# Optimization experiments

Measured on AMD Instinct MI355X. Metric: run time of the kernel, lower is better.

## Reference

```python
import jax, jax.numpy as jnp
import numpy as np

N_IN, N_HID, N_OUT = 200, 256, 2
BN_EPS = 1e-5


def _mlp(x, W1, b1, W2, b2):
    # two-layer MLP with ELU activations (dropout prob = 0.0 -> omitted)
    h = jax.nn.elu(x @ W1 + b1)
    return jax.nn.elu(h @ W2 + b2)


def _batch_norm(x, gamma, beta):
    # torch BatchNorm1d in training mode over flattened (B*E) rows, biased variance
    m = x.mean(axis=(0, 1))
    v = x.var(axis=(0, 1))
    return (x - m) * jax.lax.rsqrt(v + BN_EPS) * gamma + beta


def setup_inputs() -> dict:
    key = jax.random.key(0)
    ks = jax.random.split(key, 12)
    B, N, T, D = 32, 100, 50, 4
    inputs = jax.random.normal(ks[0], (B, N, T, D), dtype=jnp.float32)
    # one-hot receiver/sender matrices over all N*(N-1) ordered off-diagonal pairs
    idx = np.array([(i, j) for i in range(N) for j in range(N) if i != j])
    eye = np.eye(N, dtype=np.float32)
    rel_rec = jnp.asarray(eye[idx[:, 0]])   # [E, N]
    rel_send = jnp.asarray(eye[idx[:, 1]])  # [E, N]

    def lin(k, fi, fo):  # xavier_normal weight
        std = float(np.sqrt(2.0 / (fi + fo)))
        return jax.random.normal(k, (fi, fo), dtype=jnp.float32) * std

    b = lambda n: jnp.full((n,), 0.1, dtype=jnp.float32)
    return dict(
        inputs=inputs, rel_rec=rel_rec, rel_send=rel_send,
        mlp1_W1=lin(ks[1], N_IN, N_HID), mlp1_b1=b(N_HID),
        mlp1_W2=lin(ks[2], N_HID, N_HID), mlp1_b2=b(N_HID),
        mlp2_W1=lin(ks[3], 2 * N_HID, N_HID), mlp2_b1=b(N_HID),
        mlp2_W2=lin(ks[4], N_HID, N_HID), mlp2_b2=b(N_HID),
        mlp3_W1=lin(ks[5], N_HID, N_HID), mlp3_b1=b(N_HID),
        mlp3_W2=lin(ks[6], N_HID, N_HID), mlp3_b2=b(N_HID),
        mlp4_W1=lin(ks[7], 3 * N_HID, N_HID), mlp4_b1=b(N_HID),
        mlp4_W2=lin(ks[8], N_HID, N_HID), mlp4_b2=b(N_HID),
        mlp4_bn_gamma=jnp.ones((N_HID,), jnp.float32),
        mlp4_bn_beta=jnp.zeros((N_HID,), jnp.float32),
        fc_W=lin(ks[9], N_HID, N_OUT), fc_b=b(N_OUT),
    )


def reference(inputs, rel_rec, rel_send,
              mlp1_W1, mlp1_b1, mlp1_W2, mlp1_b2,
              mlp2_W1, mlp2_b1, mlp2_W2, mlp2_b2,
              mlp3_W1, mlp3_b1, mlp3_W2, mlp3_b2,
              mlp4_W1, mlp4_b1, mlp4_W2, mlp4_b2,
              mlp4_bn_gamma, mlp4_bn_beta, fc_W, fc_b):
    B, N = inputs.shape[0], inputs.shape[1]
    x = inputs.reshape(B, N, -1)                       # [B, N, T*D]
    x = _mlp(x, mlp1_W1, mlp1_b1, mlp1_W2, mlp1_b2)     # [B, N, H]

    def node2edge(h):
        recv = jnp.einsum('en,bnh->beh', rel_rec, h)
        send = jnp.einsum('en,bnh->beh', rel_send, h)
        return jnp.concatenate([send, recv], axis=2)    # [B, E, 2H]

    x = node2edge(x)
    x = _mlp(x, mlp2_W1, mlp2_b1, mlp2_W2, mlp2_b2)     # [B, E, H]
    x_skip = x
    # factor=True branch
    incoming = jnp.einsum('en,beh->bnh', rel_rec, x) / x.shape[1]  # edge2node, /N per code
    x = _mlp(incoming, mlp3_W1, mlp3_b1, mlp3_W2, mlp3_b2)
    x = node2edge(x)                                    # [B, E, 2H]
    x = jnp.concatenate([x, x_skip], axis=2)            # [B, E, 3H]
    x = _mlp(x, mlp4_W1, mlp4_b1, mlp4_W2, mlp4_b2)
    x = _batch_norm(x, mlp4_bn_gamma, mlp4_bn_beta)
    return x @ fc_W + fc_b                              # [B, E, n_out]
```

## Files before the change

kernel.cpp:

```cpp
#include <hip/hip_runtime.h>
#include <math.h>


typedef unsigned short ushort_t;
typedef __bf16 bf16x8 __attribute__((ext_vector_type(8)));
typedef float  f32x4  __attribute__((ext_vector_type(4)));

#define E_EDGES 9900
#define NNODE   100
#define HID     256
#define M_BIG   316800
#define M_SMALL 3200
#define NBLK2   (M_BIG / 128)

__device__ __forceinline__ float bf2f(ushort_t u) {
    union { unsigned int i; float f; } v; v.i = ((unsigned int)u) << 16; return v.f;
}
__device__ __forceinline__ ushort_t f2bf(float f) {
    union { float f; unsigned int i; } v; v.f = f;
    return (ushort_t)((v.i + 0x7fffu + ((v.i >> 16) & 1u)) >> 16);
}
__device__ __forceinline__ float elu_f(float x) {
    return x > 0.f ? x : (__expf(x) - 1.f);
}

__global__ __launch_bounds__(256)
void wcvt_all(const float* __restrict__ s0, const float* __restrict__ s1,
              const float* __restrict__ s2, const float* __restrict__ s3,
              const float* __restrict__ s4, const float* __restrict__ s5,
              const float* __restrict__ s6, const float* __restrict__ s7,
              ushort_t* d0, ushort_t* d1, ushort_t* d2, ushort_t* d3,
              ushort_t* d4, ushort_t* d5, ushort_t* d6, ushort_t* d7)
{
    int bid = blockIdx.x;
    const float* S; ushort_t* D; int Kd, Kr, t;
    if      (bid < 16)  { S = s0; D = d0; Kd = 256; Kr = 200; t = bid; }
    else if (bid < 32)  { S = s1; D = d1; Kd = 256; Kr = 256; t = bid - 16; }
    else if (bid < 64)  { S = s2; D = d2; Kd = 512; Kr = 512; t = bid - 32; }
    else if (bid < 80)  { S = s3; D = d3; Kd = 256; Kr = 256; t = bid - 64; }
    else if (bid < 96)  { S = s4; D = d4; Kd = 256; Kr = 256; t = bid - 80; }
    else if (bid < 112) { S = s5; D = d5; Kd = 256; Kr = 256; t = bid - 96; }
    else if (bid < 160) { S = s6; D = d6; Kd = 768; Kr = 768; t = bid - 112; }
    else                { S = s7; D = d7; Kd = 256; Kr = 256; t = bid - 160; }
    int k0 = (t >> 2) * 64, c0 = (t & 3) * 64;
    __shared__ float Sh[64][65];
    int tid = threadIdx.x;
    #pragma unroll
    for (int i = 0; i < 16; ++i) {
        int idx = tid + i * 256;
        int kk = idx >> 6, cc = idx & 63;
        Sh[kk][cc] = (k0 + kk < Kr) ? S[(size_t)(k0 + kk) * 256 + c0 + cc] : 0.f;
    }
    __syncthreads();
    int col = tid & 63;
    int kb  = (tid >> 6) * 16;
    ushort_t* dst = D + (size_t)(c0 + col) * Kd + k0 + kb;
    #pragma unroll
    for (int jj = 0; jj < 4; ++jj) {
        ushort4 u;
        u.x = f2bf(Sh[kb + 4 * jj + 0][col]);
        u.y = f2bf(Sh[kb + 4 * jj + 1][col]);
        u.z = f2bf(Sh[kb + 4 * jj + 2][col]);
        u.w = f2bf(Sh[kb + 4 * jj + 3][col]);
        *(ushort4*)(dst + 4 * jj) = u;
    }
}

__device__ __forceinline__ void gemm32(const ushort_t S[32][264],
                                       const ushort_t* __restrict__ WT,
                                       int wstr, int kcn,
                                       int w, int ln15, int klane,
                                       f32x4 acc[2][4])
{
    #pragma unroll
    for (int r = 0; r < 2; ++r)
        #pragma unroll
        for (int c = 0; c < 4; ++c)
            acc[r][c][0] = acc[r][c][1] = acc[r][c][2] = acc[r][c][3] = 0.f;
    int wch[4];
    #pragma unroll
    for (int c = 0; c < 4; ++c) wch[c] = (w * 64 + 16 * c + ln15) * wstr;
    bf16x8 wf0[4];
    #pragma unroll
    for (int c = 0; c < 4; ++c)
        wf0[c] = *(const bf16x8*)(WT + wch[c] + klane);
    for (int kc = 0; kc < kcn; ++kc) {
        bf16x8 wf1[4];
        if (kc + 1 < kcn) {
            #pragma unroll
            for (int c = 0; c < 4; ++c)
                wf1[c] = *(const bf16x8*)(WT + wch[c] + (kc + 1) * 32 + klane);
        }
        bf16x8 af[2];
        #pragma unroll
        for (int r = 0; r < 2; ++r)
            af[r] = *(const bf16x8*)&S[16 * r + ln15][kc * 32 + klane];
        #pragma unroll
        for (int r = 0; r < 2; ++r)
            #pragma unroll
            for (int c = 0; c < 4; ++c)
                acc[r][c] = __builtin_amdgcn_mfma_f32_16x16x32_bf16(wf0[c], af[r], acc[r][c], 0, 0, 0);
        #pragma unroll
        for (int c = 0; c < 4; ++c) wf0[c] = wf1[c];
    }
}

__device__ __forceinline__ void park32(ushort_t D[32][264], f32x4 acc[2][4],
                                       const float* __restrict__ bias,
                                       int act, int w, int ln15, int q)
{
    #pragma unroll
    for (int c = 0; c < 4; ++c) {
        float4 bv = bias ? *(const float4*)&bias[w * 64 + 16 * c + 4 * q]
                         : make_float4(0.f, 0.f, 0.f, 0.f);
        #pragma unroll
        for (int r = 0; r < 2; ++r) {
            float o0 = acc[r][c][0] + bv.x;
            float o1 = acc[r][c][1] + bv.y;
            float o2 = acc[r][c][2] + bv.z;
            float o3 = acc[r][c][3] + bv.w;
            if (act) { o0 = elu_f(o0); o1 = elu_f(o1); o2 = elu_f(o2); o3 = elu_f(o3); }
            ushort4 u;
            u.x = f2bf(o0); u.y = f2bf(o1); u.z = f2bf(o2); u.w = f2bf(o3);
            *(ushort4*)&D[16 * r + ln15][w * 64 + 16 * c + 4 * q] = u;
        }
    }
}

__global__ __launch_bounds__(256, 4)
void mlp_pq(const float* __restrict__ Xf, int Kreal, int kcN, float xscale,
            const ushort_t* __restrict__ W1T, const float* __restrict__ b1,
            const ushort_t* __restrict__ W2T, const float* __restrict__ b2,
            const ushort_t* __restrict__ WPT, int wsPQ,
            const float* __restrict__ bP, ushort_t* __restrict__ Pout,
            const ushort_t* __restrict__ WQT, ushort_t* __restrict__ Qout)
{
    __shared__ ushort_t Abuf[32][264];
    __shared__ ushort_t Bbuf[32][264];
    const int tid = threadIdx.x;
    const int w = tid >> 6;
    const int l = tid & 63;
    const int ln15 = l & 15;
    const int q = l >> 4;
    const int klane = 8 * q;
    const int Rbase = blockIdx.x * 32;

    {
        int row = tid >> 3, seg = tid & 7;
        if (seg < kcN) {
            ushort_t tmp[32];
            const float* src = Xf + (size_t)(Rbase + row) * Kreal + seg * 32;
            #pragma unroll
            for (int u = 0; u < 32; ++u)
                tmp[u] = (seg * 32 + u < Kreal) ? f2bf(src[u] * xscale) : (ushort_t)0;
            #pragma unroll
            for (int u = 0; u < 4; ++u)
                *(uint4*)&Abuf[row][seg * 32 + u * 8] = *(uint4*)&tmp[u * 8];
        }
    }
    __syncthreads();

    f32x4 acc[2][4];
    gemm32(Abuf, W1T, 256, kcN, w, ln15, klane, acc);
    park32(Bbuf, acc, b1, 1, w, ln15, q);
    __syncthreads();
    gemm32(Bbuf, W2T, 256, 8, w, ln15, klane, acc);
    park32(Abuf, acc, b2, 1, w, ln15, q);
    __syncthreads();
    gemm32(Abuf, WPT, wsPQ, 8, w, ln15, klane, acc);
    park32(Bbuf, acc, bP, 0, w, ln15, q);
    __syncthreads();
    f32x4 acq[2][4];
    gemm32(Abuf, WQT, wsPQ, 8, w, ln15, klane, acq);
    #pragma unroll
    for (int m = 0; m < 4; ++m) {
        int ch = tid + m * 256;
        int row = ch >> 5;
        int o = (ch & 31) * 8;
        *(uint4*)&Pout[(size_t)(Rbase + row) * 256 + o] = *(const uint4*)&Bbuf[row][o];
    }
    __syncthreads();
    park32(Bbuf, acq, nullptr, 0, w, ln15, q);
    __syncthreads();
    #pragma unroll
    for (int m = 0; m < 4; ++m) {
        int ch = tid + m * 256;
        int row = ch >> 5;
        int o = (ch & 31) * 8;
        *(uint4*)&Qout[(size_t)(Rbase + row) * 256 + o] = *(const uint4*)&Bbuf[row][o];
    }
}

__device__ __forceinline__ void gemm128cs(const ushort_t As[128][264],
                                          const ushort_t* __restrict__ WT,
                                          int wstr, int w, int ln15, int klane,
                                          f32x4 acc[8][2])
{
    #pragma unroll
    for (int r = 0; r < 8; ++r)
        #pragma unroll
        for (int c = 0; c < 2; ++c)
            acc[r][c][0] = acc[r][c][1] = acc[r][c][2] = acc[r][c][3] = 0.f;
    int wch[2];
    #pragma unroll
    for (int c = 0; c < 2; ++c) wch[c] = (w * 32 + 16 * c + ln15) * wstr;
    bf16x8 wf0[2];
    #pragma unroll
    for (int c = 0; c < 2; ++c)
        wf0[c] = *(const bf16x8*)(WT + wch[c] + klane);
    #pragma unroll
    for (int kc = 0; kc < 8; ++kc) {
        bf16x8 wf1[2];
        if (kc < 7) {
            #pragma unroll
            for (int c = 0; c < 2; ++c)
                wf1[c] = *(const bf16x8*)(WT + wch[c] + (kc + 1) * 32 + klane);
        }
        #pragma unroll
        for (int g = 0; g < 2; ++g) {
            bf16x8 af[4];
            #pragma unroll
            for (int r = 0; r < 4; ++r)
                af[r] = *(const bf16x8*)&As[16 * (4 * g + r) + ln15][kc * 32 + klane];
            #pragma unroll
            for (int r = 0; r < 4; ++r)
                #pragma unroll
                for (int c = 0; c < 2; ++c)
                    acc[4 * g + r][c] = __builtin_amdgcn_mfma_f32_16x16x32_bf16(wf0[c], af[r], acc[4 * g + r][c], 0, 0, 0);
        }
        #pragma unroll
        for (int c = 0; c < 2; ++c) wf0[c] = wf1[c];
    }
}

__global__ __launch_bounds__(512, 4)
void edge_mlp2(const ushort_t* __restrict__ Pb, const ushort_t* __restrict__ Qb,
               const ushort_t* __restrict__ W2T,
               const float* __restrict__ b2,
               ushort_t* __restrict__ Y, float* __restrict__ aux)
{
    __shared__ ushort_t As[128][264];
    const int tid = threadIdx.x;
    const int w = tid >> 6;
    const int l = tid & 63;
    const int ln15 = l & 15;
    const int q = l >> 4;
    const int klane = 8 * q;
    const int Rbase = blockIdx.x * 128;

    {
        int row = tid >> 2;
        int R = Rbase + row;
        int b = R / E_EDGES;
        int e = R - b * E_EDGES;
        int i = e / 99;
        int k = e - 99 * i;
        int j = k + (k >= i ? 1 : 0);
        const ushort_t* prow = Pb + (size_t)(b * NNODE + j) * HID;
        const ushort_t* qrow = Qb + (size_t)(b * NNODE + i) * HID;
        int off = (tid & 3) * 8;
        uint4 pv[8], qv[8];
        #pragma unroll
        for (int u = 0; u < 8; ++u) {
            int o = off + u * 32;
            pv[u] = *(const uint4*)(prow + o);
            qv[u] = *(const uint4*)(qrow + o);
        }
        #pragma unroll
        for (int u = 0; u < 8; ++u) {
            int o = off + u * 32;
            union { uint4 v; ushort_t s[8]; } pu, qu, hu;
            pu.v = pv[u]; qu.v = qv[u];
            #pragma unroll
            for (int x = 0; x < 8; ++x)
                hu.s[x] = f2bf(elu_f(bf2f(pu.s[x]) + bf2f(qu.s[x])));
            *(uint4*)&As[row][o] = hu.v;
        }
    }
    __syncthreads();

    f32x4 acc[8][2];
    gemm128cs(As, W2T, 256, w, ln15, klane, acc);
    __syncthreads();

    #pragma unroll
    for (int c = 0; c < 2; ++c) {
        float4 bv = *(const float4*)&b2[w * 32 + 16 * c + 4 * q];
        #pragma unroll
        for (int r = 0; r < 8; ++r) {
            ushort4 u;
            u.x = f2bf(elu_f(acc[r][c][0] + bv.x));
            u.y = f2bf(elu_f(acc[r][c][1] + bv.y));
            u.z = f2bf(elu_f(acc[r][c][2] + bv.z));
            u.w = f2bf(elu_f(acc[r][c][3] + bv.w));
            *(ushort4*)&As[16 * r + ln15][w * 32 + 16 * c + 4 * q] = u;
        }
    }
    __syncthreads();

    #pragma unroll
    for (int m = 0; m < 8; ++m) {
        int ch = tid + m * 512;
        int row = ch >> 5;
        int o = (ch & 31) * 8;
        *(uint4*)&Y[((size_t)(Rbase + row)) * 256 + o] = *(const uint4*)&As[row][o];
    }

    if (tid < 64) {
        int c4 = tid * 4;
        int bn = Rbase / 99;
        int left = 99 - (Rbase - bn * 99);
        float s[4] = {0.f, 0.f, 0.f, 0.f};
        for (int r = 0; r < 128; ++r) {
            union { ushort4 v; ushort_t e[4]; } u;
            u.v = *(const ushort4*)&As[r][c4];
            #pragma unroll
            for (int g = 0; g < 4; ++g) s[g] += bf2f(u.e[g]);
            if (--left == 0) {
                #pragma unroll
                for (int g = 0; g < 4; ++g) {
                    atomicAdd(&aux[(size_t)bn * 256 + c4 + g], s[g]);
                    s[g] = 0.f;
                }
                ++bn; left = 99;
            }
        }
        #pragma unroll
        for (int g = 0; g < 4; ++g)
            atomicAdd(&aux[(size_t)bn * 256 + c4 + g], s[g]);
    }
}

__global__ __launch_bounds__(512, 4)
void edge_mlp4(const ushort_t* __restrict__ Pb, const ushort_t* __restrict__ Qb,
               const ushort_t* __restrict__ X2,
               const ushort_t* __restrict__ WaT, int wsA,
               const ushort_t* __restrict__ WbT, int wsB,
               const float* __restrict__ b2,
               ushort_t* __restrict__ Y, ushort_t* __restrict__ pstat)
{
    __shared__ ushort_t As[128][264];
    const int tid = threadIdx.x;
    const int w = tid >> 6;
    const int l = tid & 63;
    const int ln15 = l & 15;
    const int q = l >> 4;
    const int klane = 8 * q;
    const int Rbase = blockIdx.x * 128;

    {
        int row = tid >> 2;
        const ushort_t* xrow = X2 + (size_t)(Rbase + row) * 256;
        int off = (tid & 3) * 8;
        uint4 xv[8];
        #pragma unroll
        for (int u = 0; u < 8; ++u) xv[u] = *(const uint4*)(xrow + off + u * 32);
        #pragma unroll
        for (int u = 0; u < 8; ++u) *(uint4*)&As[row][off + u * 32] = xv[u];
    }

    int oP[8], oQ[8];
    #pragma unroll
    for (int r = 0; r < 8; ++r) {
        int R = Rbase + 16 * r + ln15;
        int b = R / E_EDGES;
        int e = R - b * E_EDGES;
        int i = e / 99;
        int k = e - 99 * i;
        int j = k + (k >= i ? 1 : 0);
        oP[r] = (b * NNODE + j) * HID;
        oQ[r] = (b * NNODE + i) * HID;
    }
    __syncthreads();

    f32x4 acc[8][2];
    gemm128cs(As, WaT, wsA, w, ln15, klane, acc);
    __syncthreads();

    #pragma unroll
    for (int c = 0; c < 2; ++c) {
        int ch = w * 32 + 16 * c + 4 * q;
        ushort4 pv[8], qv[8];
        #pragma unroll
        for (int r = 0; r < 8; ++r) {
            pv[r] = *(const ushort4*)(Pb + oP[r] + ch);
            qv[r] = *(const ushort4*)(Qb + oQ[r] + ch);
        }
        #pragma unroll
        for (int r = 0; r < 8; ++r) {
            union { ushort4 v; ushort_t s[4]; } pu, qu;
            pu.v = pv[r]; qu.v = qv[r];
            ushort4 u;
            u.x = f2bf(elu_f(acc[r][c][0] + bf2f(pu.s[0]) + bf2f(qu.s[0])));
            u.y = f2bf(elu_f(acc[r][c][1] + bf2f(pu.s[1]) + bf2f(qu.s[1])));
            u.z = f2bf(elu_f(acc[r][c][2] + bf2f(pu.s[2]) + bf2f(qu.s[2])));
            u.w = f2bf(elu_f(acc[r][c][3] + bf2f(pu.s[3]) + bf2f(qu.s[3])));
            *(ushort4*)&As[16 * r + ln15][ch] = u;
        }
    }
    __syncthreads();

    gemm128cs(As, WbT, wsB, w, ln15, klane, acc);
    __syncthreads();

    #pragma unroll
    for (int c = 0; c < 2; ++c) {
        float4 bv = *(const float4*)&b2[w * 32 + 16 * c + 4 * q];
        #pragma unroll
        for (int r = 0; r < 8; ++r) {
            ushort4 u;
            u.x = f2bf(elu_f(acc[r][c][0] + bv.x));
            u.y = f2bf(elu_f(acc[r][c][1] + bv.y));
            u.z = f2bf(elu_f(acc[r][c][2] + bv.z));
            u.w = f2bf(elu_f(acc[r][c][3] + bv.w));
            *(ushort4*)&As[16 * r + ln15][w * 32 + 16 * c + 4 * q] = u;
        }
    }
    __syncthreads();

    #pragma unroll
    for (int m = 0; m < 8; ++m) {
        int ch = tid + m * 512;
        int row = ch >> 5;
        int o = (ch & 31) * 8;
        *(uint4*)&Y[((size_t)(Rbase + row)) * 256 + o] = *(const uint4*)&As[row][o];
    }

    if (tid < 64) {
        int c4 = tid * 4;
        float s[4] = {0.f, 0.f, 0.f, 0.f};
        float qq[4] = {0.f, 0.f, 0.f, 0.f};
        for (int r = 0; r < 128; ++r) {
            union { ushort4 v; ushort_t e[4]; } u;
            u.v = *(const ushort4*)&As[r][c4];
            #pragma unroll
            for (int g = 0; g < 4; ++g) {
                float v = bf2f(u.e[g]);
                s[g] += v;
                qq[g] = fmaf(v, v, qq[g]);
            }
        }
        size_t base = (size_t)blockIdx.x * 512;
        ushort4 us, uq;
        us.x = f2bf(s[0]);  us.y = f2bf(s[1]);  us.z = f2bf(s[2]);  us.w = f2bf(s[3]);
        uq.x = f2bf(qq[0]); uq.y = f2bf(qq[1]); uq.z = f2bf(qq[2]); uq.w = f2bf(qq[3]);
        *(ushort4*)&pstat[base + c4]       = us;
        *(ushort4*)&pstat[base + 256 + c4] = uq;
    }
}

__global__ __launch_bounds__(256)
void reduce_stats(const ushort_t* __restrict__ pstat, float* __restrict__ stats)
{
    int c = threadIdx.x;
    float s = 0.f, q = 0.f;
    for (int b = blockIdx.x; b < NBLK2; b += 64) {
        size_t base = (size_t)b * 512;
        s += bf2f(pstat[base + c]);
        q += bf2f(pstat[base + 256 + c]);
    }
    atomicAdd(&stats[c], s);
    atomicAdd(&stats[256 + c], q);
}

__global__ __launch_bounds__(256)
void fold_kernel(const float* __restrict__ stats,
                 const float* __restrict__ gamma, const float* __restrict__ beta,
                 const float* __restrict__ fcW, const float* __restrict__ fcb,
                 float* __restrict__ fold)
{
    __shared__ float red0[256], red1[256];
    int c = threadIdx.x;
    float mean  = stats[c] * (1.f / M_BIG);
    float var   = stats[256 + c] * (1.f / M_BIG) - mean * mean;
    float inv   = rsqrtf(var + 1e-5f);
    float scale = inv * gamma[c];
    float sh    = beta[c] - mean * scale;
    float w0 = fcW[c * 2 + 0], w1 = fcW[c * 2 + 1];
    fold[c * 2 + 0] = scale * w0;
    fold[c * 2 + 1] = scale * w1;
    red0[c] = sh * w0;
    red1[c] = sh * w1;
    __syncthreads();
    for (int off = 128; off > 0; off >>= 1) {
        if (c < off) { red0[c] += red0[c + off]; red1[c] += red1[c + off]; }
        __syncthreads();
    }
    if (c == 0) {
        fold[512] = red0[0] + fcb[0];
        fold[513] = red1[0] + fcb[1];
    }
}

__global__ __launch_bounds__(256)
void final_kernel(const ushort_t* __restrict__ x4, const float* __restrict__ fold,
                  float* __restrict__ out)
{
    int tid  = threadIdx.x;
    int l32  = tid & 31;
    int g    = tid >> 5;
    int R = blockIdx.x * 8 + g;
    int c0 = l32 * 8;
    union { uint4 qv; ushort_t s[8]; } u;
    u.qv = *(const uint4*)(x4 + (size_t)R * 256 + c0);
    float a0 = 0.f, a1 = 0.f;
    #pragma unroll
    for (int j = 0; j < 8; ++j) {
        float v = bf2f(u.s[j]);
        a0 = fmaf(v, fold[(c0 + j) * 2 + 0], a0);
        a1 = fmaf(v, fold[(c0 + j) * 2 + 1], a1);
    }
    #pragma unroll
    for (int off = 16; off > 0; off >>= 1) {
        a0 += __shfl_down(a0, off);
        a1 += __shfl_down(a1, off);
    }
    if (l32 == 0) {
        out[(size_t)R * 2 + 0] = a0 + fold[512];
        out[(size_t)R * 2 + 1] = a1 + fold[513];
    }
}

extern "C" void kernel_launch(void* const* d_in, const int* in_sizes, int n_in,
                              void* d_out, int out_size, void* d_ws, size_t ws_size,
                              hipStream_t stream)
{
    (void)in_sizes; (void)n_in; (void)out_size; (void)ws_size;

    const float* inputs = (const float*)d_in[0];
    const float* m1W1 = (const float*)d_in[3];
    const float* m1b1 = (const float*)d_in[4];
    const float* m1W2 = (const float*)d_in[5];
    const float* m1b2 = (const float*)d_in[6];
    const float* m2W1 = (const float*)d_in[7];
    const float* m2b1 = (const float*)d_in[8];
    const float* m2W2 = (const float*)d_in[9];
    const float* m2b2 = (const float*)d_in[10];
    const float* m3W1 = (const float*)d_in[11];
    const float* m3b1 = (const float*)d_in[12];
    const float* m3W2 = (const float*)d_in[13];
    const float* m3b2 = (const float*)d_in[14];
    const float* m4W1 = (const float*)d_in[15];
    const float* m4b1 = (const float*)d_in[16];
    const float* m4W2 = (const float*)d_in[17];
    const float* m4b2 = (const float*)d_in[18];
    const float* gamma = (const float*)d_in[19];
    const float* beta  = (const float*)d_in[20];
    const float* fcW   = (const float*)d_in[21];
    const float* fcb   = (const float*)d_in[22];
    float* out = (float*)d_out;

    char* ws = (char*)d_ws;
    const size_t BIGB = (size_t)M_BIG * 256 * 2;
    const size_t HB   = (size_t)M_SMALL * 256 * 2;
    const size_t SM4  = (size_t)M_SMALL * 256 * 4;
    ushort_t* bigX     = (ushort_t*)ws;
    ushort_t* pstat    = (ushort_t*)(ws + BIGB);
    float*    incoming = (float*)(ws + BIGB + 2 * HB);
    ushort_t* Pbuf     = (ushort_t*)(ws + BIGB + 2 * HB + SM4);
    ushort_t* Qbuf     = (ushort_t*)(ws + BIGB + 3 * HB + SM4);
    float*    stats    = (float*)(ws + BIGB + 4 * HB + SM4);
    float*    fold     = stats + 512;
    ushort_t* w1t      = (ushort_t*)(ws + BIGB + 4 * HB + SM4 + 8192);
    ushort_t* w1bt     = w1t  + 256 * 256;
    ushort_t* w2pt     = w1bt + 256 * 256;
    ushort_t* w2t      = w2pt + 256 * 512;
    ushort_t* w3at     = w2t  + 256 * 256;
    ushort_t* w3bt     = w3at + 256 * 256;
    ushort_t* w4pt     = w3bt + 256 * 256;
    ushort_t* w4bt     = w4pt + 256 * 768;

    hipMemsetAsync(stats, 0, 2048, stream);
    hipMemsetAsync(incoming, 0, SM4, stream);

    dim3 blk(256);
    dim3 blk512(512);
    wcvt_all<<<176, blk, 0, stream>>>(m1W1, m1W2, m2W1, m2W2, m3W1, m3W2, m4W1, m4W2,
                                      w1t, w1bt, w2pt, w2t, w3at, w3bt, w4pt, w4bt);
    mlp_pq<<<100, blk, 0, stream>>>(inputs, 200, 7, 1.f,
                                    w1t, m1b1, w1bt, m1b2,
                                    w2pt, 512, m2b1, Pbuf,
                                    w2pt + 256, Qbuf);
    edge_mlp2<<<NBLK2, blk512, 0, stream>>>(Pbuf, Qbuf, w2t, m2b2, bigX, incoming);
    mlp_pq<<<100, blk, 0, stream>>>(incoming, 256, 8, 1.f / 9900.f,
                                    w3at, m3b1, w3bt, m3b2,
                                    w4pt, 768, m4b1, Pbuf,
                                    w4pt + 256, Qbuf);
    edge_mlp4<<<NBLK2, blk512, 0, stream>>>(Pbuf, Qbuf, bigX,
                                            w4pt + 512, 768, w4bt, 256,
                                            m4b2, bigX, pstat);
    reduce_stats<<<64, blk, 0, stream>>>(pstat, stats);
    fold_kernel<<<1, blk, 0, stream>>>(stats, gamma, beta, fcW, fcb, fold);
    final_kernel<<<M_BIG / 8, blk, 0, stream>>>(bigX, fold, out);
}
```

Before: 497.1 us.

## Shrink edge-MLP tiles to 64 rows with 2x4 wave grid and fused BN stats

Changes both edge MLP kernels from 128-row to 64-row tiles with a 2x4 wave arrangement (each wave owns 32 rows by 64 columns), halving LDS use and raising the occupancy target to 6 blocks per CU. Batch-norm statistics are now reduced in shared memory and atomically added in fp32 into 64 buckets, which removes the separate reduce_stats kernel and the bf16 rounding of partial sums. The float-to-bf16 helper now uses the native __bf16 conversion. The trade is more blocks and more weight reloads per row against better occupancy and one fewer launch.

New measurement: 743.0 us. 1.49x slower.

```diff
diff --git a/kernel.cpp b/kernel.cpp
--- a/kernel.cpp
+++ b/kernel.cpp
@@ -11,14 +11,13 @@
 #define HID     256
 #define M_BIG   316800
 #define M_SMALL 3200
-#define NBLK2   (M_BIG / 128)
+#define NBLK_E  (M_BIG / 64)
 
 __device__ __forceinline__ float bf2f(ushort_t u) {
     union { unsigned int i; float f; } v; v.i = ((unsigned int)u) << 16; return v.f;
 }
 __device__ __forceinline__ ushort_t f2bf(float f) {
-    union { float f; unsigned int i; } v; v.f = f;
-    return (ushort_t)((v.i + 0x7fffu + ((v.i >> 16) & 1u)) >> 16);
+    union { __bf16 h; ushort_t u; } v; v.h = (__bf16)f; return v.u;
 }
 __device__ __forceinline__ float elu_f(float x) {
     return x > 0.f ? x : (__expf(x) - 1.f);
@@ -191,131 +190,125 @@
     }
 }
 
-__device__ __forceinline__ void gemm128cs(const ushort_t As[128][264],
-                                          const ushort_t* __restrict__ WT,
-                                          int wstr, int w, int ln15, int klane,
-                                          f32x4 acc[8][2])
-{
-    #pragma unroll
-    for (int r = 0; r < 8; ++r)
-        #pragma unroll
-        for (int c = 0; c < 2; ++c)
+__device__ __forceinline__ void gemm64(const ushort_t As[64][264],
+                                       const ushort_t* __restrict__ WT,
+                                       int wstr, int wr, int wc,
+                                       int ln15, int klane,
+                                       f32x4 acc[2][4])
+{
+    #pragma unroll
+    for (int r = 0; r < 2; ++r)
+        #pragma unroll
+        for (int c = 0; c < 4; ++c)
             acc[r][c][0] = acc[r][c][1] = acc[r][c][2] = acc[r][c][3] = 0.f;
-    int wch[2];
-    #pragma unroll
-    for (int c = 0; c < 2; ++c) wch[c] = (w * 32 + 16 * c + ln15) * wstr;
-    bf16x8 wf0[2];
-    #pragma unroll
-    for (int c = 0; c < 2; ++c)
+    int wch[4];
+    #pragma unroll
+    for (int c = 0; c < 4; ++c) wch[c] = (wc * 64 + 16 * c + ln15) * wstr;
+    bf16x8 wf0[4];
+    #pragma unroll
+    for (int c = 0; c < 4; ++c)
         wf0[c] = *(const bf16x8*)(WT + wch[c] + klane);
     #pragma unroll
     for (int kc = 0; kc < 8; ++kc) {
-        bf16x8 wf1[2];
+        bf16x8 wf1[4];
         if (kc < 7) {
             #pragma unroll
-            for (int c = 0; c < 2; ++c)
+            for (int c = 0; c < 4; ++c)
                 wf1[c] = *(const bf16x8*)(WT + wch[c] + (kc + 1) * 32 + klane);
         }
-        #pragma unroll
-        for (int g = 0; g < 2; ++g) {
-            bf16x8 af[4];
-            #pragma unroll
-            for (int r = 0; r < 4; ++r)
-                af[r] = *(const bf16x8*)&As[16 * (4 * g + r) + ln15][kc * 32 + klane];
-            #pragma unroll
-            for (int r = 0; r < 4; ++r)
-                #pragma unroll
-                for (int c = 0; c < 2; ++c)
-                    acc[4 * g + r][c] = __builtin_amdgcn_mfma_f32_16x16x32_bf16(wf0[c], af[r], acc[4 * g + r][c], 0, 0, 0);
-        }
-        #pragma unroll
-        for (int c = 0; c < 2; ++c) wf0[c] = wf1[c];
-    }
-}
-
-__global__ __launch_bounds__(512, 4)
+        bf16x8 af[2];
+        #pragma unroll
+        for (int r = 0; r < 2; ++r)
+            af[r] = *(const bf16x8*)&As[wr * 32 + 16 * r + ln15][kc * 32 + klane];
+        #pragma unroll
+        for (int r = 0; r < 2; ++r)
+            #pragma unroll
+            for (int c = 0; c < 4; ++c)
+                acc[r][c] = __builtin_amdgcn_mfma_f32_16x16x32_bf16(wf0[c], af[r], acc[r][c], 0, 0, 0);
+        #pragma unroll
+        for (int c = 0; c < 2; ++c) ;
+        #pragma unroll
+        for (int c = 0; c < 4; ++c) wf0[c] = wf1[c];
+    }
+}
+
+__global__ __launch_bounds__(512, 6)
 void edge_mlp2(const ushort_t* __restrict__ Pb, const ushort_t* __restrict__ Qb,
                const ushort_t* __restrict__ W2T,
                const float* __restrict__ b2,
                ushort_t* __restrict__ Y, float* __restrict__ aux)
 {
-    __shared__ ushort_t As[128][264];
+    __shared__ ushort_t As[64][264];
     const int tid = threadIdx.x;
     const int w = tid >> 6;
     const int l = tid & 63;
     const int ln15 = l & 15;
     const int q = l >> 4;
     const int klane = 8 * q;
-    const int Rbase = blockIdx.x * 128;
-
-    {
-        int row = tid >> 2;
+    const int wr = w >> 2;
+    const int wc = w & 3;
+    const int Rbase = blockIdx.x * 64;
+
+    #pragma unroll
+    for (int m = 0; m < 4; ++m) {
+        int ch = tid + m * 512;
+        int row = ch >> 5;
+        int co = (ch & 31) * 8;
         int R = Rbase + row;
         int b = R / E_EDGES;
         int e = R - b * E_EDGES;
         int i = e / 99;
         int k = e - 99 * i;
         int j = k + (k >= i ? 1 : 0);
-        const ushort_t* prow = Pb + (size_t)(b * NNODE + j) * HID;
-        const ushort_t* qrow = Qb + (size_t)(b * NNODE + i) * HID;
-        int off = (tid & 3) * 8;
-        uint4 pv[8], qv[8];
-        #pragma unroll
-        for (int u = 0; u < 8; ++u) {
-            int o = off + u * 32;
-            pv[u] = *(const uint4*)(prow + o);
-            qv[u] = *(const uint4*)(qrow + o);
-        }
-        #pragma unroll
-        for (int u = 0; u < 8; ++u) {
-            int o = off + u * 32;
-            union { uint4 v; ushort_t s[8]; } pu, qu, hu;
-            pu.v = pv[u]; qu.v = qv[u];
-            #pragma unroll
-            for (int x = 0; x < 8; ++x)
-                hu.s[x] = f2bf(elu_f(bf2f(pu.s[x]) + bf2f(qu.s[x])));
-            *(uint4*)&As[row][o] = hu.v;
-        }
-    }
-    __syncthreads();
-
-    f32x4 acc[8][2];
-    gemm128cs(As, W2T, 256, w, ln15, klane, acc);
-    __syncthreads();
-
-    #pragma unroll
-    for (int c = 0; c < 2; ++c) {
-        float4 bv = *(const float4*)&b2[w * 32 + 16 * c + 4 * q];
-        #pragma unroll
-        for (int r = 0; r < 8; ++r) {
+        union { uint4 v; ushort_t s[8]; } pu, qu, hu;
+        pu.v = *(const uint4*)(Pb + (size_t)(b * NNODE + j) * HID + co);
+        qu.v = *(const uint4*)(Qb + (size_t)(b * NNODE + i) * HID + co);
+        #pragma unroll
+        for (int x = 0; x < 8; ++x)
+            hu.s[x] = f2bf(elu_f(bf2f(pu.s[x]) + bf2f(qu.s[x])));
+        *(uint4*)&As[row][co] = hu.v;
+    }
+    __syncthreads();
+
+    f32x4 acc[2][4];
+    gemm64(As, W2T, 256, wr, wc, ln15, klane, acc);
+    __syncthreads();
+
+    #pragma unroll
+    for (int c = 0; c < 4; ++c) {
+        float4 bv = *(const float4*)&b2[wc * 64 + 16 * c + 4 * q];
+        #pragma unroll
+        for (int r = 0; r < 2; ++r) {
             ushort4 u;
             u.x = f2bf(elu_f(acc[r][c][0] + bv.x));
             u.y = f2bf(elu_f(acc[r][c][1] + bv.y));
             u.z = f2bf(elu_f(acc[r][c][2] + bv.z));
             u.w = f2bf(elu_f(acc[r][c][3] + bv.w));
-            *(ushort4*)&As[16 * r + ln15][w * 32 + 16 * c + 4 * q] = u;
-        }
-    }
-    __syncthreads();
-
-    #pragma unroll
-    for (int m = 0; m < 8; ++m) {
+            *(ushort4*)&As[wr * 32 + 16 * r + ln15][wc * 64 + 16 * c + 4 * q] = u;
+        }
+    }
+    __syncthreads();
+
+    #pragma unroll
+    for (int m = 0; m < 4; ++m) {
         int ch = tid + m * 512;
         int row = ch >> 5;
         int o = (ch & 31) * 8;
         *(uint4*)&Y[((size_t)(Rbase + row)) * 256 + o] = *(const uint4*)&As[row][o];
     }
 
-    if (tid < 64) {
-        int c4 = tid * 4;
-        int bn = Rbase / 99;
-        int left = 99 - (Rbase - bn * 99);
+    if (w < 4) {
+        int c4 = l * 4;
+        int r0 = w * 16;
+        int R0 = Rbase + r0;
+        int bn = R0 / 99;
+        int left = 99 - (R0 - bn * 99);
         float s[4] = {0.f, 0.f, 0.f, 0.f};
-        for (int r = 0; r < 128; ++r) {
-            union { ushort4 v; ushort_t e[4]; } u;
+        for (int r = r0; r < r0 + 16; ++r) {
+            union { ushort4 v; ushort_t e4[4]; } u;
             u.v = *(const ushort4*)&As[r][c4];
             #pragma unroll
-            for (int g = 0; g < 4; ++g) s[g] += bf2f(u.e[g]);
+            for (int g = 0; g < 4; ++g) s[g] += bf2f(u.e4[g]);
             if (--left == 0) {
                 #pragma unroll
                 for (int g = 0; g < 4; ++g) {
@@ -325,44 +318,51 @@
                 ++bn; left = 99;
             }
         }
-        #pragma unroll
-        for (int g = 0; g < 4; ++g)
-            atomicAdd(&aux[(size_t)bn * 256 + c4 + g], s[g]);
-    }
-}
-
-__global__ __launch_bounds__(512, 4)
+        if (left != 99) {
+            #pragma unroll
+            for (int g = 0; g < 4; ++g)
+                atomicAdd(&aux[(size_t)bn * 256 + c4 + g], s[g]);
+        }
+    }
+}
+
+__global__ __launch_bounds__(512, 6)
 void edge_mlp4(const ushort_t* __restrict__ Pb, const ushort_t* __restrict__ Qb,
                const ushort_t* __restrict__ X2,
                const ushort_t* __restrict__ WaT, int wsA,
                const ushort_t* __restrict__ WbT, int wsB,
                const float* __restrict__ b2,
-               ushort_t* __restrict__ Y, ushort_t* __restrict__ pstat)
-{
-    __shared__ ushort_t As[128][264];
+               ushort_t* __restrict__ Y, float* __restrict__ pbuck)
+{
+    __shared__ ushort_t As[64][264];
+    __shared__ float Sc[4][512];
     const int tid = threadIdx.x;
     const int w = tid >> 6;
     const int l = tid & 63;
     const int ln15 = l & 15;
     const int q = l >> 4;
     const int klane = 8 * q;
-    const int Rbase = blockIdx.x * 128;
-
-    {
-        int row = tid >> 2;
-        const ushort_t* xrow = X2 + (size_t)(Rbase + row) * 256;
-        int off = (tid & 3) * 8;
-        uint4 xv[8];
-        #pragma unroll
-        for (int u = 0; u < 8; ++u) xv[u] = *(const uint4*)(xrow + off + u * 32);
-        #pragma unroll
-        for (int u = 0; u < 8; ++u) *(uint4*)&As[row][off + u * 32] = xv[u];
-    }
-
-    int oP[8], oQ[8];
-    #pragma unroll
-    for (int r = 0; r < 8; ++r) {
-        int R = Rbase + 16 * r + ln15;
+    const int wr = w >> 2;
+    const int wc = w & 3;
+    const int Rbase = blockIdx.x * 64;
+
+    #pragma unroll
+    for (int m = 0; m < 4; ++m) {
+        int ch = tid + m * 512;
+        int row = ch >> 5;
+        int o = (ch & 31) * 8;
+        *(uint4*)&As[row][o] = *(const uint4*)(X2 + (size_t)(Rbase + row) * 256 + o);
+    }
+    __syncthreads();
+
+    f32x4 acc[2][4];
+    gemm64(As, WaT, wsA, wr, wc, ln15, klane, acc);
+    __syncthreads();
+
+    int oP[2], oQ[2];
+    #pragma unroll
+    for (int r = 0; r < 2; ++r) {
+        int R = Rbase + wr * 32 + 16 * r + ln15;
         int b = R / E_EDGES;
         int e = R - b * E_EDGES;
         int i = e / 99;
@@ -371,108 +371,98 @@
         oP[r] = (b * NNODE + j) * HID;
         oQ[r] = (b * NNODE + i) * HID;
     }
-    __syncthreads();
-
-    f32x4 acc[8][2];
-    gemm128cs(As, WaT, wsA, w, ln15, klane, acc);
-    __syncthreads();
-
-    #pragma unroll
-    for (int c = 0; c < 2; ++c) {
-        int ch = w * 32 + 16 * c + 4 * q;
-        ushort4 pv[8], qv[8];
-        #pragma unroll
-        for (int r = 0; r < 8; ++r) {
-            pv[r] = *(const ushort4*)(Pb + oP[r] + ch);
-            qv[r] = *(const ushort4*)(Qb + oQ[r] + ch);
-        }
-        #pragma unroll
-        for (int r = 0; r < 8; ++r) {
-            union { ushort4 v; ushort_t s[4]; } pu, qu;
-            pu.v = pv[r]; qu.v = qv[r];
+
+    #pragma unroll
+    for (int c = 0; c < 4; ++c) {
+        int chn = wc * 64 + 16 * c + 4 * q;
+        #pragma unroll
+        for (int r = 0; r < 2; ++r) {
+            union { ushort4 v; ushort_t s4[4]; } pu, qu;
+            pu.v = *(const ushort4*)(Pb + oP[r] + chn);
+            qu.v = *(const ushort4*)(Qb + oQ[r] + chn);
             ushort4 u;
-            u.x = f2bf(elu_f(acc[r][c][0] + bf2f(pu.s[0]) + bf2f(qu.s[0])));
-            u.y = f2bf(elu_f(acc[r][c][1] + bf2f(pu.s[1]) + bf2f(qu.s[1])));
-            u.z = f2bf(elu_f(acc[r][c][2] + bf2f(pu.s[2]) + bf2f(qu.s[2])));
-            u.w = f2bf(elu_f(acc[r][c][3] + bf2f(pu.s[3]) + bf2f(qu.s[3])));
-            *(ushort4*)&As[16 * r + ln15][ch] = u;
-        }
-    }
-    __syncthreads();
-
-    gemm128cs(As, WbT, wsB, w, ln15, klane, acc);
-    __syncthreads();
-
-    #pragma unroll
-    for (int c = 0; c < 2; ++c) {
-        float4 bv = *(const float4*)&b2[w * 32 + 16 * c + 4 * q];
-        #pragma unroll
-        for (int r = 0; r < 8; ++r) {
+            u.x = f2bf(elu_f(acc[r][c][0] + bf2f(pu.s4[0]) + bf2f(qu.s4[0])));
+            u.y = f2bf(elu_f(acc[r][c][1] + bf2f(pu.s4[1]) + bf2f(qu.s4[1])));
+            u.z = f2bf(elu_f(acc[r][c][2] + bf2f(pu.s4[2]) + bf2f(qu.s4[2])));
+            u.w = f2bf(elu_f(acc[r][c][3] + bf2f(pu.s4[3]) + bf2f(qu.s4[3])));
+            *(ushort4*)&As[wr * 32 + 16 * r + ln15][chn] = u;
+        }
+    }
+    __syncthreads();
+
+    gemm64(As, WbT, wsB, wr, wc, ln15, klane, acc);
+    __syncthreads();
+
+    #pragma unroll
+    for (int c = 0; c < 4; ++c) {
+        float4 bv = *(const float4*)&b2[wc * 64 + 16 * c + 4 * q];
+        #pragma unroll
+        for (int r = 0; r < 2; ++r) {
             ushort4 u;
             u.x = f2bf(elu_f(acc[r][c][0] + bv.x));
             u.y = f2bf(elu_f(acc[r][c][1] + bv.y));
             u.z = f2bf(elu_f(acc[r][c][2] + bv.z));
             u.w = f2bf(elu_f(acc[r][c][3] + bv.w));
-            *(ushort4*)&As[16 * r + ln15][w * 32 + 16 * c + 4 * q] = u;
+            *(ushort4*)&As[wr * 32 + 16 * r + ln15][wc * 64 + 16 * c + 4 * q] = u;
         }
     }
     __syncthreads();
 
     #pragma unroll
     for (int m = 0; m < 8; ++m) {
+        int ch = tid + m * 512;
+        int row = ch >> 6;
+        (void)row;
+    }
+    #pragma unroll
+    for (int m = 0; m < 4; ++m) {
         int ch = tid + m * 512;
         int row = ch >> 5;
         int o = (ch & 31) * 8;
         *(uint4*)&Y[((size_t)(Rbase + row)) * 256 + o] = *(const uint4*)&As[row][o];
     }
 
-    if (tid < 64) {
-        int c4 = tid * 4;
-        float s[4] = {0.f, 0.f, 0.f, 0.f};
-        float qq[4] = {0.f, 0.f, 0.f, 0.f};
-        for (int r = 0; r < 128; ++r) {
-            union { ushort4 v; ushort_t e[4]; } u;
+    if (w < 4) {
+        int c4 = l * 4;
+        float s[4] = {0.f, 0.f, 0.f, 0.f}, qq[4] = {0.f, 0.f, 0.f, 0.f};
+        for (int r = w * 16; r < w * 16 + 16; ++r) {
+            union { ushort4 v; ushort_t e4[4]; } u;
             u.v = *(const ushort4*)&As[r][c4];
             #pragma unroll
             for (int g = 0; g < 4; ++g) {
-                float v = bf2f(u.e[g]);
+                float v = bf2f(u.e4[g]);
                 s[g] += v;
                 qq[g] = fmaf(v, v, qq[g]);
             }
         }
-        size_t base = (size_t)blockIdx.x * 512;
-        ushort4 us, uq;
-        us.x = f2bf(s[0]);  us.y = f2bf(s[1]);  us.z = f2bf(s[2]);  us.w = f2bf(s[3]);
-        uq.x = f2bf(qq[0]); uq.y = f2bf(qq[1]); uq.z = f2bf(qq[2]); uq.w = f2bf(qq[3]);
-        *(ushort4*)&pstat[base + c4]       = us;
-        *(ushort4*)&pstat[base + 256 + c4] = uq;
+        #pragma unroll
+        for (int g = 0; g < 4; ++g) {
+            Sc[w][c4 + g]       = s[g];
+            Sc[w][256 + c4 + g] = qq[g];
+        }
+    }
+    __syncthreads();
+    {
+        float v = Sc[0][tid] + Sc[1][tid] + Sc[2][tid] + Sc[3][tid];
+        atomicAdd(&pbuck[((size_t)(blockIdx.x & 63) << 9) + tid], v);
     }
 }
 
 __global__ __launch_bounds__(256)
-void reduce_stats(const ushort_t* __restrict__ pstat, float* __restrict__ stats)
-{
-    int c = threadIdx.x;
-    float s = 0.f, q = 0.f;
-    for (int b = blockIdx.x; b < NBLK2; b += 64) {
-        size_t base = (size_t)b * 512;
-        s += bf2f(pstat[base + c]);
-        q += bf2f(pstat[base + 256 + c]);
-    }
-    atomicAdd(&stats[c], s);
-    atomicAdd(&stats[256 + c], q);
-}
-
-__global__ __launch_bounds__(256)
-void fold_kernel(const float* __restrict__ stats,
+void fold_kernel(const float* __restrict__ pbuck,
                  const float* __restrict__ gamma, const float* __restrict__ beta,
                  const float* __restrict__ fcW, const float* __restrict__ fcb,
                  float* __restrict__ fold)
 {
     __shared__ float red0[256], red1[256];
     int c = threadIdx.x;
-    float mean  = stats[c] * (1.f / M_BIG);
-    float var   = stats[256 + c] * (1.f / M_BIG) - mean * mean;
+    float s = 0.f, qsum = 0.f;
+    for (int k = 0; k < 64; ++k) {
+        s    += pbuck[k * 512 + c];
+        qsum += pbuck[k * 512 + 256 + c];
+    }
+    float mean  = s * (1.f / M_BIG);
+    float var   = qsum * (1.f / M_BIG) - mean * mean;
     float inv   = rsqrtf(var + 1e-5f);
     float scale = inv * gamma[c];
     float sh    = beta[c] - mean * scale;
@@ -552,16 +542,16 @@
 
     char* ws = (char*)d_ws;
     const size_t BIGB = (size_t)M_BIG * 256 * 2;
+    const size_t PB   = 64 * 512 * 4;
     const size_t HB   = (size_t)M_SMALL * 256 * 2;
     const size_t SM4  = (size_t)M_SMALL * 256 * 4;
     ushort_t* bigX     = (ushort_t*)ws;
-    ushort_t* pstat    = (ushort_t*)(ws + BIGB);
-    float*    incoming = (float*)(ws + BIGB + 2 * HB);
-    ushort_t* Pbuf     = (ushort_t*)(ws + BIGB + 2 * HB + SM4);
-    ushort_t* Qbuf     = (ushort_t*)(ws + BIGB + 3 * HB + SM4);
-    float*    stats    = (float*)(ws + BIGB + 4 * HB + SM4);
-    float*    fold     = stats + 512;
-    ushort_t* w1t      = (ushort_t*)(ws + BIGB + 4 * HB + SM4 + 8192);
+    float*    pbuck    = (float*)(ws + BIGB);
+    float*    incoming = (float*)(ws + BIGB + PB);
+    ushort_t* Pbuf     = (ushort_t*)(ws + BIGB + PB + SM4);
+    ushort_t* Qbuf     = (ushort_t*)(ws + BIGB + PB + SM4 + HB);
+    float*    fold     = (float*)(ws + BIGB + PB + SM4 + 2 * HB);
+    ushort_t* w1t      = (ushort_t*)(ws + BIGB + PB + SM4 + 2 * HB + 4096);
     ushort_t* w1bt     = w1t  + 256 * 256;
     ushort_t* w2pt     = w1bt + 256 * 256;
     ushort_t* w2t      = w2pt + 256 * 512;
@@ -570,7 +560,7 @@
     ushort_t* w4pt     = w3bt + 256 * 256;
     ushort_t* w4bt     = w4pt + 256 * 768;
 
-    hipMemsetAsync(stats, 0, 2048, stream);
+    hipMemsetAsync(pbuck, 0, PB, stream);
     hipMemsetAsync(incoming, 0, SM4, stream);
 
     dim3 blk(256);
@@ -581,15 +571,14 @@
                                     w1t, m1b1, w1bt, m1b2,
                                     w2pt, 512, m2b1, Pbuf,
                                     w2pt + 256, Qbuf);
-    edge_mlp2<<<NBLK2, blk512, 0, stream>>>(Pbuf, Qbuf, w2t, m2b2, bigX, incoming);
+    edge_mlp2<<<NBLK_E, blk512, 0, stream>>>(Pbuf, Qbuf, w2t, m2b2, bigX, incoming);
     mlp_pq<<<100, blk, 0, stream>>>(incoming, 256, 8, 1.f / 9900.f,
                                     w3at, m3b1, w3bt, m3b2,
                                     w4pt, 768, m4b1, Pbuf,
                                     w4pt + 256, Qbuf);
-    edge_mlp4<<<NBLK2, blk512, 0, stream>>>(Pbuf, Qbuf, bigX,
-                                            w4pt + 512, 768, w4bt, 256,
-                                            m4b2, bigX, pstat);
-    reduce_stats<<<64, blk, 0, stream>>>(pstat, stats);
-    fold_kernel<<<1, blk, 0, stream>>>(stats, gamma, beta, fcW, fcb, fold);
+    edge_mlp4<<<NBLK_E, blk512, 0, stream>>>(Pbuf, Qbuf, bigX,
+                                             w4pt + 512, 768, w4bt, 256,
+                                             m4b2, bigX, pbuck);
+    fold_kernel<<<1, blk, 0, stream>>>(pbuck, gamma, beta, fcW, fcb, fold);
     final_kernel<<<M_BIG / 8, blk, 0, stream>>>(bigX, fold, out);
 }
```

## Replace edge-sum atomics with two-buffer partial stores and parallelize BN stats

Applied to the files above, without the earlier changes.

Edge-to-node sums in edge_mlp2 now go out as plain stores into two partial buffers instead of float atomics. A node's 99 edges span at most two 128-row blocks, so each block writes its leading partial node to a second buffer. The next mlp_pq adds the two buffers while loading. edge_mlp4's per-block column statistics are now split over four waves and combined through shared memory, in place of a single wave walking all 128 rows. f2bf is switched to the compiler's __bf16 conversion. The cost is an extra buffer read in mlp_pq and a reused workspace region that must be zeroed.

Measured after the change: 471.5 us. -5.1%, faster.

```diff
diff --git a/kernel.cpp b/kernel.cpp
--- a/kernel.cpp
+++ b/kernel.cpp
@@ -17,8 +17,7 @@
     union { unsigned int i; float f; } v; v.i = ((unsigned int)u) << 16; return v.f;
 }
 __device__ __forceinline__ ushort_t f2bf(float f) {
-    union { float f; unsigned int i; } v; v.f = f;
-    return (ushort_t)((v.i + 0x7fffu + ((v.i >> 16) & 1u)) >> 16);
+    union { __bf16 h; ushort_t u; } v; v.h = (__bf16)f; return v.u;
 }
 __device__ __forceinline__ float elu_f(float x) {
     return x > 0.f ? x : (__expf(x) - 1.f);
@@ -128,7 +127,8 @@
 }
 
 __global__ __launch_bounds__(256, 4)
-void mlp_pq(const float* __restrict__ Xf, int Kreal, int kcN, float xscale,
+void mlp_pq(const float* __restrict__ Xf, const float* __restrict__ Xf2,
+            int Kreal, int kcN, float xscale,
             const ushort_t* __restrict__ W1T, const float* __restrict__ b1,
             const ushort_t* __restrict__ W2T, const float* __restrict__ b2,
             const ushort_t* __restrict__ WPT, int wsPQ,
@@ -149,10 +149,18 @@
         int row = tid >> 3, seg = tid & 7;
         if (seg < kcN) {
             ushort_t tmp[32];
-            const float* src = Xf + (size_t)(Rbase + row) * Kreal + seg * 32;
-            #pragma unroll
-            for (int u = 0; u < 32; ++u)
-                tmp[u] = (seg * 32 + u < Kreal) ? f2bf(src[u] * xscale) : (ushort_t)0;
+            const float* src  = Xf + (size_t)(Rbase + row) * Kreal + seg * 32;
+            const float* src2 = Xf2 ? Xf2 + (size_t)(Rbase + row) * Kreal + seg * 32
+                                    : (const float*)nullptr;
+            #pragma unroll
+            for (int u = 0; u < 32; ++u) {
+                float a = 0.f;
+                if (seg * 32 + u < Kreal) {
+                    a = src[u];
+                    if (Xf2) a += src2[u];
+                }
+                tmp[u] = f2bf(a * xscale);
+            }
             #pragma unroll
             for (int u = 0; u < 4; ++u)
                 *(uint4*)&Abuf[row][seg * 32 + u * 8] = *(uint4*)&tmp[u * 8];
@@ -237,7 +245,8 @@
 void edge_mlp2(const ushort_t* __restrict__ Pb, const ushort_t* __restrict__ Qb,
                const ushort_t* __restrict__ W2T,
                const float* __restrict__ b2,
-               ushort_t* __restrict__ Y, float* __restrict__ aux)
+               ushort_t* __restrict__ Y,
+               float* __restrict__ part0, float* __restrict__ part1)
 {
     __shared__ ushort_t As[128][264];
     const int tid = threadIdx.x;
@@ -309,25 +318,31 @@
     if (tid < 64) {
         int c4 = tid * 4;
         int bn = Rbase / 99;
-        int left = 99 - (Rbase - bn * 99);
+        int off0 = Rbase - bn * 99;
+        int left = 99 - off0;
+        int first = 1;
         float s[4] = {0.f, 0.f, 0.f, 0.f};
         for (int r = 0; r < 128; ++r) {
-            union { ushort4 v; ushort_t e[4]; } u;
+            union { ushort4 v; ushort_t e4[4]; } u;
             u.v = *(const ushort4*)&As[r][c4];
             #pragma unroll
-            for (int g = 0; g < 4; ++g) s[g] += bf2f(u.e[g]);
+            for (int g = 0; g < 4; ++g) s[g] += bf2f(u.e4[g]);
             if (--left == 0) {
+                float* dst = (first && off0 != 0) ? part1 : part0;
                 #pragma unroll
                 for (int g = 0; g < 4; ++g) {
-                    atomicAdd(&aux[(size_t)bn * 256 + c4 + g], s[g]);
+                    dst[(size_t)bn * 256 + c4 + g] = s[g];
                     s[g] = 0.f;
                 }
-                ++bn; left = 99;
+                ++bn; left = 99; first = 0;
             }
         }
-        #pragma unroll
-        for (int g = 0; g < 4; ++g)
-            atomicAdd(&aux[(size_t)bn * 256 + c4 + g], s[g]);
+        if (left != 99) {
+            float* dst = (first && off0 != 0) ? part1 : part0;
+            #pragma unroll
+            for (int g = 0; g < 4; ++g)
+                dst[(size_t)bn * 256 + c4 + g] = s[g];
+        }
     }
 }
 
@@ -340,6 +355,7 @@
                ushort_t* __restrict__ Y, ushort_t* __restrict__ pstat)
 {
     __shared__ ushort_t As[128][264];
+    __shared__ float Sc[4][512];
     const int tid = threadIdx.x;
     const int w = tid >> 6;
     const int l = tid & 63;
@@ -426,26 +442,30 @@
         *(uint4*)&Y[((size_t)(Rbase + row)) * 256 + o] = *(const uint4*)&As[row][o];
     }
 
-    if (tid < 64) {
-        int c4 = tid * 4;
+    if (w < 4) {
+        int c4 = l * 4;
         float s[4] = {0.f, 0.f, 0.f, 0.f};
         float qq[4] = {0.f, 0.f, 0.f, 0.f};
-        for (int r = 0; r < 128; ++r) {
-            union { ushort4 v; ushort_t e[4]; } u;
+        for (int r = w * 32; r < w * 32 + 32; ++r) {
+            union { ushort4 v; ushort_t e4[4]; } u;
             u.v = *(const ushort4*)&As[r][c4];
             #pragma unroll
             for (int g = 0; g < 4; ++g) {
-                float v = bf2f(u.e[g]);
+                float v = bf2f(u.e4[g]);
                 s[g] += v;
                 qq[g] = fmaf(v, v, qq[g]);
             }
         }
-        size_t base = (size_t)blockIdx.x * 512;
-        ushort4 us, uq;
-        us.x = f2bf(s[0]);  us.y = f2bf(s[1]);  us.z = f2bf(s[2]);  us.w = f2bf(s[3]);
-        uq.x = f2bf(qq[0]); uq.y = f2bf(qq[1]); uq.z = f2bf(qq[2]); uq.w = f2bf(qq[3]);
-        *(ushort4*)&pstat[base + c4]       = us;
-        *(ushort4*)&pstat[base + 256 + c4] = uq;
+        #pragma unroll
+        for (int g = 0; g < 4; ++g) {
+            Sc[w][c4 + g]       = s[g];
+            Sc[w][256 + c4 + g] = qq[g];
+        }
+    }
+    __syncthreads();
+    {
+        float v = Sc[0][tid] + Sc[1][tid] + Sc[2][tid] + Sc[3][tid];
+        pstat[(size_t)blockIdx.x * 512 + tid] = f2bf(v);
     }
 }
 
@@ -556,7 +576,8 @@
     const size_t SM4  = (size_t)M_SMALL * 256 * 4;
     ushort_t* bigX     = (ushort_t*)ws;
     ushort_t* pstat    = (ushort_t*)(ws + BIGB);
-    float*    incoming = (float*)(ws + BIGB + 2 * HB);
+    float*    part1    = (float*)(ws + BIGB);
+    float*    part0    = (float*)(ws + BIGB + 2 * HB);
     ushort_t* Pbuf     = (ushort_t*)(ws + BIGB + 2 * HB + SM4);
     ushort_t* Qbuf     = (ushort_t*)(ws + BIGB + 3 * HB + SM4);
     float*    stats    = (float*)(ws + BIGB + 4 * HB + SM4);
@@ -571,18 +592,18 @@
     ushort_t* w4bt     = w4pt + 256 * 768;
 
     hipMemsetAsync(stats, 0, 2048, stream);
-    hipMemsetAsync(incoming, 0, SM4, stream);
+    hipMemsetAsync(part1, 0, SM4, stream);
 
     dim3 blk(256);
     dim3 blk512(512);
     wcvt_all<<<176, blk, 0, stream>>>(m1W1, m1W2, m2W1, m2W2, m3W1, m3W2, m4W1, m4W2,
                                       w1t, w1bt, w2pt, w2t, w3at, w3bt, w4pt, w4bt);
-    mlp_pq<<<100, blk, 0, stream>>>(inputs, 200, 7, 1.f,
+    mlp_pq<<<100, blk, 0, stream>>>(inputs, nullptr, 200, 7, 1.f,
                                     w1t, m1b1, w1bt, m1b2,
                                     w2pt, 512, m2b1, Pbuf,
                                     w2pt + 256, Qbuf);
-    edge_mlp2<<<NBLK2, blk512, 0, stream>>>(Pbuf, Qbuf, w2t, m2b2, bigX, incoming);
-    mlp_pq<<<100, blk, 0, stream>>>(incoming, 256, 8, 1.f / 9900.f,
+    edge_mlp2<<<NBLK2, blk512, 0, stream>>>(Pbuf, Qbuf, w2t, m2b2, bigX, part0, part1);
+    mlp_pq<<<100, blk, 0, stream>>>(part0, part1, 256, 8, 1.f / 9900.f,
                                     w3at, m3b1, w3bt, m3b2,
                                     w4pt, 768, m4b1, Pbuf,
                                     w4pt + 256, Qbuf);
```
